# Kernel optimization log

Hardware: AMD Instinct MI355X
Metric: run time of the kernel (lower is better)

## Reference

```python
import jax, jax.numpy as jnp
import numpy as np

INP_DIM = 1024
PROJ_DIM = 1024
SEQ = 2048
BATCH = 4

def setup_inputs() -> dict:
    key = jax.random.key(0)
    k1, k2, k3, k4 = jax.random.split(key, 4)
    inputs = jax.random.normal(k1, (BATCH, SEQ, INP_DIM), dtype=jnp.float32)
    # nn.Linear weights stored as (out, in); we keep them that way and transpose in matmul
    Wq = jax.random.normal(k2, (PROJ_DIM, INP_DIM), dtype=jnp.float32) * (1.0 / np.sqrt(INP_DIM))
    Wk = jax.random.normal(k3, (PROJ_DIM, INP_DIM), dtype=jnp.float32) * (1.0 / np.sqrt(INP_DIM))
    Wv = jax.random.normal(k4, (PROJ_DIM, INP_DIM), dtype=jnp.float32) * (1.0 / np.sqrt(INP_DIM))
    return {"inputs": inputs, "Wq": Wq, "Wk": Wk, "Wv": Wv}

def reference(inputs, Wq, Wk, Wv):
    # QKV projections: x @ W.T (nn.Linear convention)
    Q = jnp.einsum('bsd,pd->bsp', inputs, Wq)
    K = jnp.einsum('bsd,pd->bsp', inputs, Wk)
    V = jnp.einsum('bsd,pd->bsp', inputs, Wv)
    scores = jnp.einsum('bqp,bkp->bqk', Q, K)  # [B, S, S]
    n = inputs.shape[1]
    causal = jnp.tril(jnp.ones((n, n), dtype=bool))  # True = keep
    scores = jnp.where(causal, scores, -jnp.inf)
    weights = jax.nn.softmax(scores / jnp.sqrt(jnp.float32(Q.shape[-1])), axis=-1)
    # dropout rate = 0.0 -> identity
    Z = jnp.einsum('bqk,bkp->bqp', weights, V)
    return Z
```

## Files before the change

kernel.cpp:

```cpp
#include <hip/hip_runtime.h>
#include <stdint.h>

#define SEQ   2048
#define DIM   1024
#define BATCH 4

typedef _Float16 f16;
typedef __attribute__((ext_vector_type(8))) _Float16 f16x8;
typedef __attribute__((ext_vector_type(4))) _Float16 f16x4;
typedef __attribute__((ext_vector_type(4))) float   f32x4;

typedef void __attribute__((address_space(1))) vg_t;
typedef void __attribute__((address_space(3))) vl_t;

__device__ __forceinline__ void gld16(const void* g, void* l) {
  __builtin_amdgcn_global_load_lds((vg_t*)g, (vl_t*)l, 16, 0, 0);
}

__global__ __launch_bounds__(256) void cvt_f32_f16(const float* __restrict__ in,
                                                   f16* __restrict__ out, int n) {
  int i = (blockIdx.x * 256 + threadIdx.x) * 4;
  if (i < n) {
    float4 v = *(const float4*)(in + i);
    f16x4 o = { (f16)v.x, (f16)v.y, (f16)v.z, (f16)v.w };
    *(f16x4*)(out + i) = o;
  }
}

template <int MODE, int CAUSAL>
__global__ __launch_bounds__(256) void gemm_bt(const f16* __restrict__ A, int lda, long aOffZ,
                                               const f16* __restrict__ B, int ldb, long bOffZ,
                                               void* __restrict__ Cv, int ldc, long cOffZ,
                                               int K) {
  __shared__ __align__(16) f16 lA[128 * 64];
  __shared__ __align__(16) f16 lB[128 * 64];

  const int tid  = threadIdx.x;
  const int wave = tid >> 6;
  const int lane = tid & 63;
  const int m0 = blockIdx.x * 128;
  const int n0 = blockIdx.y * 128;
  const int z  = blockIdx.z;

  if (CAUSAL == 1 && n0 >= m0 + 128) return;
  const int Keff = (CAUSAL == 2) ? (m0 + 128) : K;

  const f16* Ab = A + (long)z * aOffZ + (long)m0 * lda;
  const f16* Bb = B + (long)z * bOffZ + (long)n0 * ldb;

  const int wm = (wave & 1) * 64;
  const int wn = (wave >> 1) * 64;

  f32x4 acc[4][4] = {};

  const int srow = lane >> 3;
  const int sj   = lane & 7;
  const int fr   = lane & 15;
  const int fq   = lane >> 4;

  for (int kt = 0; kt < Keff; kt += 64) {
    __syncthreads();
#pragma unroll
    for (int j = 0; j < 4; ++j) {
      const int rgrp = j * 4 + wave;
      const int row  = rgrp * 8 + srow;
      const int gch  = sj ^ (row & 7);
      gld16(Ab + (long)row * lda + kt + gch * 8, (void*)(lA + rgrp * 512 + lane * 8));
      gld16(Bb + (long)row * ldb + kt + gch * 8, (void*)(lB + rgrp * 512 + lane * 8));
    }
    __syncthreads();

#pragma unroll
    for (int kk = 0; kk < 64; kk += 32) {
      f16x8 af[4], bf[4];
#pragma unroll
      for (int i = 0; i < 4; ++i) {
        const int arow = wm + i * 16 + fr;
        const int ach  = (kk / 8 + fq) ^ (arow & 7);
        af[i] = *(const f16x8*)(lA + arow * 64 + ach * 8);
        const int brow = wn + i * 16 + fr;
        const int bch  = (kk / 8 + fq) ^ (brow & 7);
        bf[i] = *(const f16x8*)(lB + brow * 64 + bch * 8);
      }
#pragma unroll
      for (int mi = 0; mi < 4; ++mi)
#pragma unroll
        for (int ni = 0; ni < 4; ++ni)
          acc[mi][ni] = __builtin_amdgcn_mfma_f32_16x16x32_f16(af[mi], bf[ni], acc[mi][ni], 0, 0, 0);
    }
  }

#pragma unroll
  for (int mi = 0; mi < 4; ++mi) {
    const int row = m0 + wm + mi * 16 + fq * 4;
#pragma unroll
    for (int ni = 0; ni < 4; ++ni) {
      const int col = n0 + wn + ni * 16 + fr;
      if constexpr (MODE == 0) {
        float* C = (float*)Cv + (long)z * cOffZ;
#pragma unroll
        for (int r = 0; r < 4; ++r) C[(long)(row + r) * ldc + col] = acc[mi][ni][r];
      } else if constexpr (MODE == 1) {
        f16* C = (f16*)Cv + (long)z * cOffZ;
#pragma unroll
        for (int r = 0; r < 4; ++r) C[(long)(row + r) * ldc + col] = (f16)acc[mi][ni][r];
      } else {
        f16* C = (f16*)Cv + (long)z * cOffZ;
        f16x4 o = { (f16)acc[mi][ni][0], (f16)acc[mi][ni][1],
                    (f16)acc[mi][ni][2], (f16)acc[mi][ni][3] };
        *(f16x4*)(C + (long)col * ldc + row) = o;
      }
    }
  }
}

__global__ __launch_bounds__(256) void softmax_causal(float* S) {
  const int q = blockIdx.x, b = blockIdx.y;
  float* row = S + ((long)b * SEQ + q) * SEQ;
  f16* prow = (f16*)row;
  const int tid = threadIdx.x;
  const int lane = tid & 63, wave = tid >> 6;
  const int nvalid = q + 1;

  float v[8];
  float m = -3.0e38f;
#pragma unroll
  for (int i = 0; i < 8; ++i) {
    const int k = tid + i * 256;
    v[i] = (k < nvalid) ? row[k] * 0.03125f : -3.0e38f;
    m = fmaxf(m, v[i]);
  }
#pragma unroll
  for (int off = 32; off; off >>= 1) m = fmaxf(m, __shfl_xor(m, off));
  __shared__ float redm[4], reds[4];
  if (lane == 0) redm[wave] = m;
  __syncthreads();
  m = fmaxf(fmaxf(redm[0], redm[1]), fmaxf(redm[2], redm[3]));

  float s = 0.f;
#pragma unroll
  for (int i = 0; i < 8; ++i) {
    const float p = (v[i] > -1.0e37f) ? __expf(v[i] - m) : 0.f;
    v[i] = p;
    s += p;
  }
#pragma unroll
  for (int off = 32; off; off >>= 1) s += __shfl_xor(s, off);
  if (lane == 0) reds[wave] = s;
  __syncthreads();
  s = reds[0] + reds[1] + reds[2] + reds[3];
  const float inv = 1.f / s;
#pragma unroll
  for (int i = 0; i < 8; ++i) {
    const int k = tid + i * 256;
    prow[k] = (f16)(v[i] * inv);
  }
}

extern "C" void kernel_launch(void* const* d_in, const int* in_sizes, int n_in,
                              void* d_out, int out_size, void* d_ws, size_t ws_size,
                              hipStream_t stream) {
  const float* x  = (const float*)d_in[0];
  const float* Wq = (const float*)d_in[1];
  const float* Wk = (const float*)d_in[2];
  const float* Wv = (const float*)d_in[3];
  float* out = (float*)d_out;

  if (ws_size < 140509184u) return;

  f16* xb = (f16*)d_ws;
  f16* Wh = xb + (size_t)8 * 1024 * 1024;
  f16* Qh = Wh + (size_t)3 * 1024 * 1024;
  f16* Kh = Qh + (size_t)8 * 1024 * 1024;
  f16* VT = Kh + (size_t)8 * 1024 * 1024;
  float* Sc = (float*)(VT + (size_t)8 * 1024 * 1024);

  const long QOFF = (long)SEQ * DIM;
  const long SOFF = (long)SEQ * SEQ;

  cvt_f32_f16<<<8192, 256, 0, stream>>>(x, xb, BATCH * SEQ * DIM);
  cvt_f32_f16<<<1024, 256, 0, stream>>>(Wq, Wh, DIM * DIM);
  cvt_f32_f16<<<1024, 256, 0, stream>>>(Wk, Wh + (size_t)DIM * DIM, DIM * DIM);
  cvt_f32_f16<<<1024, 256, 0, stream>>>(Wv, Wh + (size_t)2 * DIM * DIM, DIM * DIM);

  gemm_bt<1, 0><<<dim3(64, 8, 1), 256, 0, stream>>>(xb, DIM, 0, Wh, DIM, 0, Qh, DIM, 0, DIM);
  gemm_bt<1, 0><<<dim3(64, 8, 1), 256, 0, stream>>>(xb, DIM, 0, Wh + (size_t)DIM * DIM, DIM, 0, Kh, DIM, 0, DIM);
  gemm_bt<2, 0><<<dim3(64, 8, 1), 256, 0, stream>>>(xb, DIM, 0, Wh + (size_t)2 * DIM * DIM, DIM, 0, VT, BATCH * SEQ, 0, DIM);

  gemm_bt<0, 1><<<dim3(16, 16, 4), 256, 0, stream>>>(Qh, DIM, QOFF, Kh, DIM, QOFF, Sc, SEQ, SOFF, DIM);

  softmax_causal<<<dim3(SEQ, BATCH), 256, 0, stream>>>(Sc);

  gemm_bt<0, 2><<<dim3(16, 8, 4), 256, 0, stream>>>((const f16*)Sc, 2 * SEQ, (long)SEQ * 2 * SEQ,
                                                    VT, BATCH * SEQ, SEQ,
                                                    out, DIM, (long)SEQ * DIM, SEQ);
}
```

Baseline: 276.8 us.

## Fuse conversions and QKV GEMMs, store scores in fp16, widen K tile

Merges the four f32-to-f16 conversion launches into one kernel and the three projection GEMMs into a single 24-column-tile launch whose epilogue routes output to Q, K or transposed V. Writes the causal score matrix in fp16 instead of fp32, which halves score traffic and lets softmax use vectorized 8-element loads and stores with a contiguous per-thread layout. Makes the GEMM K-tile a template parameter and uses 128 for the attention GEMMs. Scores rounded to fp16 before scaling lose some precision, and the larger LDS tiles may reduce occupancy.

```diff
diff --git a/kernel.cpp b/kernel.cpp
--- a/kernel.cpp
+++ b/kernel.cpp
@@ -17,23 +17,34 @@
   __builtin_amdgcn_global_load_lds((vg_t*)g, (vl_t*)l, 16, 0, 0);
 }
 
-__global__ __launch_bounds__(256) void cvt_f32_f16(const float* __restrict__ in,
-                                                   f16* __restrict__ out, int n) {
-  int i = (blockIdx.x * 256 + threadIdx.x) * 4;
-  if (i < n) {
-    float4 v = *(const float4*)(in + i);
-    f16x4 o = { (f16)v.x, (f16)v.y, (f16)v.z, (f16)v.w };
-    *(f16x4*)(out + i) = o;
-  }
-}
-
-template <int MODE, int CAUSAL>
+__global__ __launch_bounds__(256) void cvt_all(const float* __restrict__ x,
+                                               const float* __restrict__ wq,
+                                               const float* __restrict__ wk,
+                                               const float* __restrict__ wv,
+                                               f16* __restrict__ xb,
+                                               f16* __restrict__ wh) {
+  const int bx = blockIdx.x;
+  const float* in; f16* out; int base;
+  if (bx < 8192)       { in = x;  out = xb;             base = bx; }
+  else if (bx < 9216)  { in = wq; out = wh;             base = bx - 8192; }
+  else if (bx < 10240) { in = wk; out = wh + (1 << 20); base = bx - 9216; }
+  else                 { in = wv; out = wh + (2 << 20); base = bx - 10240; }
+  const long i = ((long)base * 256 + threadIdx.x) * 4;
+  float4 v = *(const float4*)(in + i);
+  f16x4 o = { (f16)v.x, (f16)v.y, (f16)v.z, (f16)v.w };
+  *(f16x4*)(out + i) = o;
+}
+
+template <int MODE, int CAUSAL, int BK>
 __global__ __launch_bounds__(256) void gemm_bt(const f16* __restrict__ A, int lda, long aOffZ,
                                                const f16* __restrict__ B, int ldb, long bOffZ,
                                                void* __restrict__ Cv, int ldc, long cOffZ,
                                                int K) {
-  __shared__ __align__(16) f16 lA[128 * 64];
-  __shared__ __align__(16) f16 lB[128 * 64];
+  constexpr int CH  = BK / 8;
+  constexpr int RPL = 64 / CH;
+  constexpr int NL  = 32 / RPL;
+  __shared__ __align__(16) f16 lA[128 * BK];
+  __shared__ __align__(16) f16 lB[128 * BK];
 
   const int tid  = threadIdx.x;
   const int wave = tid >> 6;
@@ -53,34 +64,34 @@
 
   f32x4 acc[4][4] = {};
 
-  const int srow = lane >> 3;
-  const int sj   = lane & 7;
+  const int srow = lane / CH;
+  const int sj   = lane % CH;
   const int fr   = lane & 15;
   const int fq   = lane >> 4;
 
-  for (int kt = 0; kt < Keff; kt += 64) {
+  for (int kt = 0; kt < Keff; kt += BK) {
     __syncthreads();
 #pragma unroll
-    for (int j = 0; j < 4; ++j) {
+    for (int j = 0; j < NL; ++j) {
       const int rgrp = j * 4 + wave;
-      const int row  = rgrp * 8 + srow;
-      const int gch  = sj ^ (row & 7);
+      const int row  = rgrp * RPL + srow;
+      const int gch  = sj ^ (row & (CH - 1));
       gld16(Ab + (long)row * lda + kt + gch * 8, (void*)(lA + rgrp * 512 + lane * 8));
       gld16(Bb + (long)row * ldb + kt + gch * 8, (void*)(lB + rgrp * 512 + lane * 8));
     }
     __syncthreads();
 
 #pragma unroll
-    for (int kk = 0; kk < 64; kk += 32) {
+    for (int kk = 0; kk < BK; kk += 32) {
       f16x8 af[4], bf[4];
 #pragma unroll
       for (int i = 0; i < 4; ++i) {
         const int arow = wm + i * 16 + fr;
-        const int ach  = (kk / 8 + fq) ^ (arow & 7);
-        af[i] = *(const f16x8*)(lA + arow * 64 + ach * 8);
+        const int ach  = (kk / 8 + fq) ^ (arow & (CH - 1));
+        af[i] = *(const f16x8*)(lA + arow * BK + ach * 8);
         const int brow = wn + i * 16 + fr;
-        const int bch  = (kk / 8 + fq) ^ (brow & 7);
-        bf[i] = *(const f16x8*)(lB + brow * 64 + bch * 8);
+        const int bch  = (kk / 8 + fq) ^ (brow & (CH - 1));
+        bf[i] = *(const f16x8*)(lB + brow * BK + bch * 8);
       }
 #pragma unroll
       for (int mi = 0; mi < 4; ++mi)
@@ -104,30 +115,45 @@
         f16* C = (f16*)Cv + (long)z * cOffZ;
 #pragma unroll
         for (int r = 0; r < 4; ++r) C[(long)(row + r) * ldc + col] = (f16)acc[mi][ni][r];
-      } else {
+      } else if constexpr (MODE == 2) {
         f16* C = (f16*)Cv + (long)z * cOffZ;
         f16x4 o = { (f16)acc[mi][ni][0], (f16)acc[mi][ni][1],
                     (f16)acc[mi][ni][2], (f16)acc[mi][ni][3] };
         *(f16x4*)(C + (long)col * ldc + row) = o;
+      } else {
+        f16* Qh  = (f16*)Cv;
+        f16* Kh  = Qh + (size_t)8 * 1024 * 1024;
+        f16* VTb = Kh + (size_t)8 * 1024 * 1024;
+        if (col < 1024) {
+#pragma unroll
+          for (int r = 0; r < 4; ++r) Qh[(long)(row + r) * DIM + col] = (f16)acc[mi][ni][r];
+        } else if (col < 2048) {
+#pragma unroll
+          for (int r = 0; r < 4; ++r) Kh[(long)(row + r) * DIM + (col - 1024)] = (f16)acc[mi][ni][r];
+        } else {
+          f16x4 o = { (f16)acc[mi][ni][0], (f16)acc[mi][ni][1],
+                      (f16)acc[mi][ni][2], (f16)acc[mi][ni][3] };
+          *(f16x4*)(VTb + (long)(col - 2048) * (BATCH * SEQ) + row) = o;
+        }
       }
     }
   }
 }
 
-__global__ __launch_bounds__(256) void softmax_causal(float* S) {
+__global__ __launch_bounds__(256) void softmax_causal(f16* S) {
   const int q = blockIdx.x, b = blockIdx.y;
-  float* row = S + ((long)b * SEQ + q) * SEQ;
-  f16* prow = (f16*)row;
+  f16* row = S + ((long)b * SEQ + q) * SEQ;
   const int tid = threadIdx.x;
   const int lane = tid & 63, wave = tid >> 6;
   const int nvalid = q + 1;
 
+  f16x8 vv = *(const f16x8*)(row + tid * 8);
   float v[8];
   float m = -3.0e38f;
 #pragma unroll
   for (int i = 0; i < 8; ++i) {
-    const int k = tid + i * 256;
-    v[i] = (k < nvalid) ? row[k] * 0.03125f : -3.0e38f;
+    const int k = tid * 8 + i;
+    v[i] = (k < nvalid) ? (float)vv[i] * 0.03125f : -3.0e38f;
     m = fmaxf(m, v[i]);
   }
 #pragma unroll
@@ -150,11 +176,10 @@
   __syncthreads();
   s = reds[0] + reds[1] + reds[2] + reds[3];
   const float inv = 1.f / s;
-#pragma unroll
-  for (int i = 0; i < 8; ++i) {
-    const int k = tid + i * 256;
-    prow[k] = (f16)(v[i] * inv);
-  }
+  f16x8 o;
+#pragma unroll
+  for (int i = 0; i < 8; ++i) o[i] = (f16)(v[i] * inv);
+  *(f16x8*)(row + tid * 8) = o;
 }
 
 extern "C" void kernel_launch(void* const* d_in, const int* in_sizes, int n_in,
@@ -166,32 +191,28 @@
   const float* Wv = (const float*)d_in[3];
   float* out = (float*)d_out;
 
-  if (ws_size < 140509184u) return;
+  if (ws_size < (size_t)51 * 1024 * 1024 * 2) return;
 
   f16* xb = (f16*)d_ws;
   f16* Wh = xb + (size_t)8 * 1024 * 1024;
   f16* Qh = Wh + (size_t)3 * 1024 * 1024;
   f16* Kh = Qh + (size_t)8 * 1024 * 1024;
   f16* VT = Kh + (size_t)8 * 1024 * 1024;
-  float* Sc = (float*)(VT + (size_t)8 * 1024 * 1024);
+  f16* Sc = VT + (size_t)8 * 1024 * 1024;
 
   const long QOFF = (long)SEQ * DIM;
   const long SOFF = (long)SEQ * SEQ;
 
-  cvt_f32_f16<<<8192, 256, 0, stream>>>(x, xb, BATCH * SEQ * DIM);
-  cvt_f32_f16<<<1024, 256, 0, stream>>>(Wq, Wh, DIM * DIM);
-  cvt_f32_f16<<<1024, 256, 0, stream>>>(Wk, Wh + (size_t)DIM * DIM, DIM * DIM);
-  cvt_f32_f16<<<1024, 256, 0, stream>>>(Wv, Wh + (size_t)2 * DIM * DIM, DIM * DIM);
-
-  gemm_bt<1, 0><<<dim3(64, 8, 1), 256, 0, stream>>>(xb, DIM, 0, Wh, DIM, 0, Qh, DIM, 0, DIM);
-  gemm_bt<1, 0><<<dim3(64, 8, 1), 256, 0, stream>>>(xb, DIM, 0, Wh + (size_t)DIM * DIM, DIM, 0, Kh, DIM, 0, DIM);
-  gemm_bt<2, 0><<<dim3(64, 8, 1), 256, 0, stream>>>(xb, DIM, 0, Wh + (size_t)2 * DIM * DIM, DIM, 0, VT, BATCH * SEQ, 0, DIM);
-
-  gemm_bt<0, 1><<<dim3(16, 16, 4), 256, 0, stream>>>(Qh, DIM, QOFF, Kh, DIM, QOFF, Sc, SEQ, SOFF, DIM);
+  cvt_all<<<11264, 256, 0, stream>>>(x, Wq, Wk, Wv, xb, Wh);
+
+  gemm_bt<3, 0, 64><<<dim3(64, 24, 1), 256, 0, stream>>>(xb, DIM, 0, Wh, DIM, 0, Qh, 0, 0, DIM);
+
+  gemm_bt<1, 1, 128><<<dim3(16, 16, 4), 256, 0, stream>>>(Qh, DIM, QOFF, Kh, DIM, QOFF,
+                                                          Sc, SEQ, SOFF, DIM);
 
   softmax_causal<<<dim3(SEQ, BATCH), 256, 0, stream>>>(Sc);
 
-  gemm_bt<0, 2><<<dim3(16, 8, 4), 256, 0, stream>>>((const f16*)Sc, 2 * SEQ, (long)SEQ * 2 * SEQ,
-                                                    VT, BATCH * SEQ, SEQ,
-                                                    out, DIM, (long)SEQ * DIM, SEQ);
-}
+  gemm_bt<0, 2, 128><<<dim3(16, 8, 4), 256, 0, stream>>>(Sc, SEQ, SOFF,
+                                                         VT, BATCH * SEQ, SEQ,
+                                                         out, DIM, (long)SEQ * DIM, SEQ);
+}
```

Result: faster. 244.4 us (-11.7%).
